# Optimization experiments

Measured on AMD Instinct MI355X. Metric: run time of the kernel, lower is better.

## Reference

```python
import jax, jax.numpy as jnp
import numpy as np

B, S_T, S_S, P, D = 4, 8, 4, 1024, 1024
NUM_REF = 256
NUM_SHARED = 256
TOPK = 4
TEMP = 1.0
STUDENT_FRAMES = [0, 2, 4, 6]          # teacher indices used by student
EXTRA_FRAMES = [1, 3, 5, 7]            # teacher-only frames
SHARED_TEACHER = [2, 4, 6]             # shared frames (student_frame_indices[1:])
W_D1 = W_D2 = W_D3 = 1.0
HUBER_OUTER_BETA = 0.5


def setup_inputs() -> dict:
    key = jax.random.key(0)
    k1, k2, k3, k4 = jax.random.split(key, 4)
    teacher_feats = jax.random.normal(k1, (B, S_T, P, D), dtype=jnp.float32)
    student_feats = jax.random.normal(k2, (B, S_S, P, D), dtype=jnp.float32)
    ref_perm = jax.random.randint(k3, (NUM_REF,), 0, P, dtype=jnp.int32)
    shared_perm = jax.random.randint(k4, (NUM_SHARED,), 0, P, dtype=jnp.int32)
    return {"teacher_feats": teacher_feats, "student_feats": student_feats,
            "ref_perm": ref_perm, "shared_perm": shared_perm}


def _l2_normalize(x, eps=1e-12):
    n = jnp.maximum(jnp.linalg.norm(x, axis=-1, keepdims=True), eps)
    return x / n


def _smooth_l1_zero(x, beta):
    # SmoothL1Loss(x, 0) elementwise
    ax = jnp.abs(x)
    return jnp.where(ax < beta, 0.5 * ax * ax / beta, ax - 0.5 * beta)


def _kl_branch(diff_t, diff_s):
    # KL(softmax(diff_t/T) || softmax(diff_s/T)) over last dim, then outer huber vs 0
    log_p = jax.nn.log_softmax(diff_t / TEMP, axis=-1)
    log_q = jax.nn.log_softmax(diff_s / TEMP, axis=-1)
    kl = jnp.sum(jnp.exp(log_p) * (log_p - log_q), axis=-1)
    return jnp.sum(_smooth_l1_zero(kl, HUBER_OUTER_BETA)), kl.size


def reference(teacher_feats, student_feats, ref_perm, shared_perm):
    sg = jax.lax.stop_gradient
    N = min(NUM_REF, NUM_SHARED)

    # ref frame (teacher idx 0 -> student idx 0), subsampled patches
    ref_t = sg(teacher_feats[:, 0][:, ref_perm, :])          # [B, num_ref, D]
    ref_s = student_feats[:, 0][:, ref_perm, :]

    # teacher-only frames concatenated along patch dim: [B, 4*P, D]
    extra_t = sg(teacher_feats[:, jnp.array(EXTRA_FRAMES)].reshape(B, len(EXTRA_FRAMES) * P, D))

    # cosine-similarity top-k search (selection_mode='topk')
    sim = jnp.einsum('bnd,bmd->bnm', _l2_normalize(ref_t), _l2_normalize(extra_t))
    _, topk_idx = jax.lax.top_k(sim, TOPK)                    # [B, num_ref, topk]
    sim_high = jax.vmap(lambda e, i: e[i])(extra_t, topk_idx)  # [B, num_ref, topk, D]
    sim_high = sg(sim_high)

    rt = ref_t[:, :N, :]
    rs = ref_s[:, :N, :]
    sh = sim_high[:, :N, :, :]

    sum_d1 = jnp.float32(0.0); sum_d2 = jnp.float32(0.0); sum_d3 = jnp.float32(0.0)
    n_d1 = 0; n_d2 = 0; n_d3 = 0

    for t_idx in SHARED_TEACHER:
        s_idx = STUDENT_FRAMES.index(t_idx)
        st = sg(teacher_feats[:, t_idx][:, shared_perm[:N], :])   # [B, N, D]
        ss = student_feats[:, s_idx][:, shared_perm[:N], :]

        # d1: ref - shared
        l1, c1 = _kl_branch(rt - st, rs - ss)
        sum_d1 += l1; n_d1 += c1
        # d2: ref - sim_high
        l2, c2 = _kl_branch(rt[:, :, None, :] - sh, rs[:, :, None, :] - sh)
        sum_d2 += l2; n_d2 += c2
        # d3: shared - sim_high
        l3, c3 = _kl_branch(st[:, :, None, :] - sh, ss[:, :, None, :] - sh)
        sum_d3 += l3; n_d3 += c3

    loss = (W_D1 * sum_d1 / n_d1 + W_D2 * sum_d2 / n_d2 + W_D3 * sum_d3 / n_d3)
    return loss
```

## Files before the change

kernel.cpp:

```cpp
#include <hip/hip_runtime.h>
#include <hip/hip_bf16.h>
#include <math.h>

#define BATCH 4

typedef __bf16 bf16x8 __attribute__((ext_vector_type(8)));
typedef float f32x4 __attribute__((ext_vector_type(4)));

#define LDSTRIDE 40

__global__ __launch_bounds__(256) void convert_kernel(const float* __restrict__ teacher,
                                                      const int* __restrict__ ref_perm,
                                                      __bf16* __restrict__ Abf,
                                                      __bf16* __restrict__ Bbf,
                                                      float* __restrict__ invnorm,
                                                      float* __restrict__ acc) {
    int blk = blockIdx.x;
    int b = blk / 4352;
    int r = blk - b * 4352;
    int t = threadIdx.x;
    if (blk == 0 && t < 4) acc[t] = 0.f;
    const float* src;
    __bf16* dst;
    bool isB = (r >= 256);
    if (!isB) {
        src = teacher + (((size_t)b * 8 + 0) * 1024 + ref_perm[r]) * 1024;
        dst = Abf + ((size_t)b * 256 + r) * 1024;
    } else {
        int m = r - 256;
        int frame = 1 + 2 * (m >> 10), p = m & 1023;
        src = teacher + (((size_t)b * 8 + frame) * 1024 + p) * 1024;
        dst = Bbf + ((size_t)b * 4096 + m) * 1024;
    }
    float4 v = ((const float4*)src)[t];
    float scale = 1.0f;
    __shared__ float red[4];
    if (isB) {
        float s = v.x * v.x + v.y * v.y + v.z * v.z + v.w * v.w;
        for (int o = 32; o > 0; o >>= 1) s += __shfl_xor(s, o);
        if ((t & 63) == 0) red[t >> 6] = s;
        __syncthreads();
        float tot = red[0] + red[1] + red[2] + red[3];
        scale = 1.0f / fmaxf(sqrtf(tot), 1e-12f);
        if (t == 0) invnorm[b * 4096 + (r - 256)] = scale;
    }
    __bf16 o4[4] = {(__bf16)(v.x * scale), (__bf16)(v.y * scale),
                    (__bf16)(v.z * scale), (__bf16)(v.w * scale)};
    ((uint2*)dst)[t] = *(uint2*)o4;
}

__global__ __launch_bounds__(512) void mfma_gemm_kernel(const __bf16* __restrict__ Abf,
                                                        const __bf16* __restrict__ Bbf,
                                                        __bf16* __restrict__ scoresb) {
    int mt = blockIdx.x;
    int nt = blockIdx.y;
    int b  = blockIdx.z;
    int t = threadIdx.x;
    int lane = t & 63, wave = t >> 6;
    int wn0 = (wave & 1) * 64;
    int wm0 = (wave >> 1) * 32;
    int l15 = lane & 15, l4 = lane >> 4;

    __shared__ __bf16 As[128 * LDSTRIDE];
    __shared__ __bf16 Bs[128 * LDSTRIDE];

    const __bf16* Ab = Abf + ((size_t)b * 256 + nt * 128) * 1024;
    const __bf16* Bb = Bbf + ((size_t)b * 4096 + mt * 128) * 1024;

    int row0 = t >> 2, kc0 = t & 3;

    f32x4 acc[4][2] = {};

    for (int k0 = 0; k0 < 1024; k0 += 32) {
        uint4 a0 = *(const uint4*)(Ab + (size_t)row0 * 1024 + k0 + kc0 * 8);
        uint4 b0 = *(const uint4*)(Bb + (size_t)row0 * 1024 + k0 + kc0 * 8);
        __syncthreads();
        *(uint4*)(As + row0 * LDSTRIDE + kc0 * 8) = a0;
        *(uint4*)(Bs + row0 * LDSTRIDE + kc0 * 8) = b0;
        __syncthreads();
        bf16x8 af[4], bfr[2];
#pragma unroll
        for (int i = 0; i < 4; i++)
            af[i] = *(const bf16x8*)(As + (wn0 + i * 16 + l15) * LDSTRIDE + l4 * 8);
#pragma unroll
        for (int j = 0; j < 2; j++)
            bfr[j] = *(const bf16x8*)(Bs + (wm0 + j * 16 + l15) * LDSTRIDE + l4 * 8);
#pragma unroll
        for (int i = 0; i < 4; i++)
#pragma unroll
            for (int j = 0; j < 2; j++)
                acc[i][j] = __builtin_amdgcn_mfma_f32_16x16x32_bf16(af[i], bfr[j], acc[i][j], 0, 0, 0);
    }

    __bf16* outp = scoresb + ((size_t)b * 256 + nt * 128) * 4096 + (size_t)mt * 128;
#pragma unroll
    for (int i = 0; i < 4; i++)
#pragma unroll
        for (int j = 0; j < 2; j++)
#pragma unroll
            for (int r = 0; r < 4; r++) {
                int n = wn0 + i * 16 + l4 * 4 + r;
                int m = wm0 + j * 16 + l15;
                outp[(size_t)n * 4096 + m] = (__bf16)acc[i][j][r];
            }
}

__global__ __launch_bounds__(256) void topk_rescore_kernel(const __bf16* __restrict__ scoresb,
                                                           const float* __restrict__ teacher,
                                                           const int* __restrict__ ref_perm,
                                                           const float* __restrict__ invnorm,
                                                           int* __restrict__ topk) {
    int row = blockIdx.x;
    int b = row >> 8, n = row & 255;
    int t = threadIdx.x;
    int lane = t & 63, wave = t >> 6;

    __shared__ float refr[1024];
    __shared__ float cval[32];
    __shared__ int cidx[32];
    __shared__ int cand_i[8];
    __shared__ float exact_v[8];

    const float* Tb = teacher + (size_t)b * 8 * 1024 * 1024;
    int rp = ref_perm[n];
    ((float4*)refr)[t] = ((const float4*)(Tb + (size_t)rp * 1024))[t];

    const __bf16* srow = scoresb + (size_t)row * 4096;
    __bf16 xs[16];
    *(uint4*)xs = ((const uint4*)srow)[2 * t];
    *(uint4*)(xs + 8) = ((const uint4*)srow)[2 * t + 1];

    float v[8]; int ix[8];
#pragma unroll
    for (int i = 0; i < 8; i++) { v[i] = -1e38f; ix[i] = -1; }
#pragma unroll
    for (int jj = 0; jj < 16; jj++) {
        float xv = (float)xs[jj]; int xm = t * 16 + jj;
        if (xv > v[7]) {
            v[7] = xv; ix[7] = xm;
#pragma unroll
            for (int i = 7; i > 0; i--)
                if (v[i] > v[i - 1]) {
                    float tv = v[i]; v[i] = v[i - 1]; v[i - 1] = tv;
                    int ti = ix[i]; ix[i] = ix[i - 1]; ix[i - 1] = ti;
                }
        }
    }
    for (int r = 0; r < 8; r++) {
        float bv = v[0]; int bi = ix[0];
        for (int o = 32; o > 0; o >>= 1) {
            float ov = __shfl_xor(bv, o); int oi = __shfl_xor(bi, o);
            if (ov > bv || (ov == bv && oi > bi)) { bv = ov; bi = oi; }
        }
        if (lane == 0) { cval[wave * 8 + r] = bv; cidx[wave * 8 + r] = bi; }
        if (bi == ix[0]) {
            v[0] = v[1]; ix[0] = ix[1];
            v[1] = v[2]; ix[1] = ix[2];
            v[2] = v[3]; ix[2] = ix[3];
            v[3] = v[4]; ix[3] = ix[4];
            v[4] = v[5]; ix[4] = ix[5];
            v[5] = v[6]; ix[5] = ix[6];
            v[6] = v[7]; ix[6] = ix[7];
            v[7] = -1e38f; ix[7] = -1;
        }
    }
    __syncthreads();
    if (wave == 0) {
        float mv = (lane < 32) ? cval[lane] : -1e38f;
        int mi = (lane < 32) ? cidx[lane] : -1;
        for (int r = 0; r < 8; r++) {
            float bv = mv; int bi = mi;
            for (int o = 32; o > 0; o >>= 1) {
                float ov = __shfl_xor(bv, o); int oi = __shfl_xor(bi, o);
                if (ov > bv || (ov == bv && oi > bi)) { bv = ov; bi = oi; }
            }
            if (lane == 0) cand_i[r] = bi;
            if (bi == mi) mv = -1e38f;
        }
    }
    __syncthreads();
    for (int c = wave; c < 8; c += 4) {
        int m = cand_i[c];
        int frame = 1 + 2 * (m >> 10), p = m & 1023;
        const float* ext = Tb + ((size_t)frame * 1024 + p) * 1024;
        float s = 0.f;
#pragma unroll
        for (int jj = 0; jj < 16; jj++) {
            int d = lane + 64 * jj;
            s = fmaf(refr[d], ext[d], s);
        }
        for (int o = 32; o > 0; o >>= 1) s += __shfl_xor(s, o);
        if (lane == 0) exact_v[c] = s * invnorm[b * 4096 + m];
    }
    __syncthreads();
    if (t == 0) {
        unsigned used = 0;
        for (int r = 0; r < 4; r++) {
            float bv = -1e38f; int bc = 0;
            for (int c = 0; c < 8; c++)
                if (!(used & (1u << c)) && exact_v[c] > bv) { bv = exact_v[c]; bc = c; }
            used |= 1u << bc;
            topk[row * 4 + r] = cand_i[bc];
        }
    }
}

#define RT 0
#define RS 1024
#define ST 2048
#define SS 3072
#define SH 4096
__global__ __launch_bounds__(256) void kl_kernel(const float* __restrict__ teacher,
                                                 const float* __restrict__ student,
                                                 const int* __restrict__ ref_perm,
                                                 const int* __restrict__ shared_perm,
                                                 const int* __restrict__ topk,
                                                 float* __restrict__ acc) {
    int row = blockIdx.x;
    int ti  = blockIdx.y;
    int b = row >> 8;
    int n = row & 255;
    int t = threadIdx.x;
    int lane = t & 63, wave = t >> 6;

    __shared__ float buf[8192];
    __shared__ float res3[3];
    if (t < 3) res3[t] = 0.f;

    const float* Tb = teacher + (size_t)b * 8 * 1024 * 1024;
    const float* Sb = student + (size_t)b * 4 * 1024 * 1024;

    int rp = ref_perm[n];
    int sp = shared_perm[n];
    int t_idx = 2 * ti + 2;
    int s_idx = ti + 1;
    ((float4*)(buf + RT))[t] = ((const float4*)(Tb + (size_t)rp * 1024))[t];
    ((float4*)(buf + RS))[t] = ((const float4*)(Sb + (size_t)rp * 1024))[t];
    ((float4*)(buf + ST))[t] = ((const float4*)(Tb + ((size_t)t_idx * 1024 + sp) * 1024))[t];
    ((float4*)(buf + SS))[t] = ((const float4*)(Sb + ((size_t)s_idx * 1024 + sp) * 1024))[t];
#pragma unroll
    for (int k = 0; k < 4; k++) {
        int idx = topk[row * 4 + k];
        int frame = 1 + 2 * (idx >> 10), p = idx & 1023;
        ((float4*)(buf + SH + k * 1024))[t] = ((const float4*)(Tb + ((size_t)frame * 1024 + p) * 1024))[t];
    }
    __syncthreads();

    int nrows = (ti == 0) ? 9 : 5;
    for (int idx = wave; idx < nrows; idx += 4) {
        int r = (ti == 0) ? idx : (idx == 0 ? 0 : idx + 4);
        int at, bt, as, bs, branch;
        float w;
        if (r == 0)      { at = RT; bt = ST;                 as = RS; bs = SS; branch = 0; w = 1.f; }
        else if (r < 5)  { at = RT; bt = SH + (r - 1) * 1024; as = RS; bs = bt; branch = 1; w = 3.f; }
        else             { at = ST; bt = SH + (r - 5) * 1024; as = SS; bs = bt; branch = 2; w = 1.f; }

        float dt[16], ds[16];
        float mt = -1e38f, ms = -1e38f;
#pragma unroll
        for (int j = 0; j < 16; j++) {
            int d = lane + 64 * j;
            float av = buf[at + d], bv = buf[bt + d];
            float asv = buf[as + d], bsv = buf[bs + d];
            dt[j] = av - bv;
            ds[j] = asv - bsv;
            mt = fmaxf(mt, dt[j]);
            ms = fmaxf(ms, ds[j]);
        }
        for (int o = 32; o > 0; o >>= 1) {
            mt = fmaxf(mt, __shfl_xor(mt, o));
            ms = fmaxf(ms, __shfl_xor(ms, o));
        }
        float Zt = 0.f, Zs = 0.f, Tn = 0.f;
#pragma unroll
        for (int j = 0; j < 16; j++) {
            float et = __expf(dt[j] - mt);
            Zt += et;
            Zs += __expf(ds[j] - ms);
            Tn += et * (dt[j] - ds[j]);
        }
        for (int o = 32; o > 0; o >>= 1) {
            Zt += __shfl_xor(Zt, o);
            Zs += __shfl_xor(Zs, o);
            Tn += __shfl_xor(Tn, o);
        }
        if (lane == 0) {
            float kl = Tn / Zt - mt - __logf(Zt) + ms + __logf(Zs);
            float ax = fabsf(kl);
            float h = ax < 0.5f ? ax * ax : ax - 0.25f;
            atomicAdd(&res3[branch], h * w);
        }
    }
    __syncthreads();
    if (t < 3) atomicAdd(&acc[t], res3[t]);
}

__global__ void finalize_kernel(const float* __restrict__ acc, float* __restrict__ out) {
    out[0] = acc[0] / 3072.f + acc[1] / 12288.f + acc[2] / 12288.f;
}

extern "C" void kernel_launch(void* const* d_in, const int* in_sizes, int n_in,
                              void* d_out, int out_size, void* d_ws, size_t ws_size,
                              hipStream_t stream) {
    const float* teacher = (const float*)d_in[0];
    const float* student = (const float*)d_in[1];
    const int* ref_perm = (const int*)d_in[2];
    const int* shared_perm = (const int*)d_in[3];
    float* out = (float*)d_out;

    char* ws = (char*)d_ws;
    float* acc     = (float*)ws;
    float* invnorm = (float*)(ws + 64);
    int*   topk    = (int*)(ws + 64 + 65536);
    __bf16* Abf    = (__bf16*)(ws + 64 + 65536 + 16384);
    __bf16* Bbf    = Abf + (size_t)4 * 256 * 1024;
    __bf16* scoresb = Bbf + (size_t)4 * 4096 * 1024;

    convert_kernel<<<BATCH * 4352, 256, 0, stream>>>(teacher, ref_perm, Abf, Bbf, invnorm, acc);
    mfma_gemm_kernel<<<dim3(32, 2, 4), 512, 0, stream>>>(Abf, Bbf, scoresb);
    topk_rescore_kernel<<<1024, 256, 0, stream>>>(scoresb, teacher, ref_perm, invnorm, topk);
    kl_kernel<<<dim3(1024, 3), 256, 0, stream>>>(teacher, student, ref_perm, shared_perm, topk, acc);
    finalize_kernel<<<1, 1, 0, stream>>>(acc, out);
}
```

Before: 293.9 us.

## Fuse d2 KL branch into top-k kernel and enlarge per-wave GEMM tile

The d2 (ref minus sim_high) KL terms depend only on the ref row and its top-k neighbours, not on the shared frame. They are now computed once in the top-k kernel, using the already-loaded ref rows and weighted by 3, instead of being recomputed by the ti==0 slice of the KL kernel. That slice previously did 9 rows per block against 5 for the others, so the KL kernel becomes uniform. The GEMM also moves from 512 to 256 threads, with each wave computing a 64x64 tile (16 MFMA accumulators) and each thread loading two chunks. This gives more register reuse per LDS read but fewer waves to hide latency.

```diff
diff --git a/kernel.cpp b/kernel.cpp
--- a/kernel.cpp
+++ b/kernel.cpp
@@ -49,7 +49,7 @@
     ((uint2*)dst)[t] = *(uint2*)o4;
 }
 
-__global__ __launch_bounds__(512) void mfma_gemm_kernel(const __bf16* __restrict__ Abf,
+__global__ __launch_bounds__(256) void mfma_gemm_kernel(const __bf16* __restrict__ Abf,
                                                         const __bf16* __restrict__ Bbf,
                                                         __bf16* __restrict__ scoresb) {
     int mt = blockIdx.x;
@@ -58,7 +58,7 @@
     int t = threadIdx.x;
     int lane = t & 63, wave = t >> 6;
     int wn0 = (wave & 1) * 64;
-    int wm0 = (wave >> 1) * 32;
+    int wm0 = (wave >> 1) * 64;
     int l15 = lane & 15, l4 = lane >> 4;
 
     __shared__ __bf16 As[128 * LDSTRIDE];
@@ -67,28 +67,33 @@
     const __bf16* Ab = Abf + ((size_t)b * 256 + nt * 128) * 1024;
     const __bf16* Bb = Bbf + ((size_t)b * 4096 + mt * 128) * 1024;
 
-    int row0 = t >> 2, kc0 = t & 3;
-
-    f32x4 acc[4][2] = {};
+    int e0 = t, e1 = t + 256;
+    int row0 = e0 >> 2, kc0 = e0 & 3;
+    int row1 = e1 >> 2, kc1 = e1 & 3;
+
+    f32x4 acc[4][4] = {};
 
     for (int k0 = 0; k0 < 1024; k0 += 32) {
         uint4 a0 = *(const uint4*)(Ab + (size_t)row0 * 1024 + k0 + kc0 * 8);
+        uint4 a1 = *(const uint4*)(Ab + (size_t)row1 * 1024 + k0 + kc1 * 8);
         uint4 b0 = *(const uint4*)(Bb + (size_t)row0 * 1024 + k0 + kc0 * 8);
+        uint4 b1 = *(const uint4*)(Bb + (size_t)row1 * 1024 + k0 + kc1 * 8);
         __syncthreads();
         *(uint4*)(As + row0 * LDSTRIDE + kc0 * 8) = a0;
+        *(uint4*)(As + row1 * LDSTRIDE + kc1 * 8) = a1;
         *(uint4*)(Bs + row0 * LDSTRIDE + kc0 * 8) = b0;
+        *(uint4*)(Bs + row1 * LDSTRIDE + kc1 * 8) = b1;
         __syncthreads();
-        bf16x8 af[4], bfr[2];
+        bf16x8 af[4], bfr[4];
+#pragma unroll
+        for (int i = 0; i < 4; i++) {
+            af[i]  = *(const bf16x8*)(As + (wn0 + i * 16 + l15) * LDSTRIDE + l4 * 8);
+            bfr[i] = *(const bf16x8*)(Bs + (wm0 + i * 16 + l15) * LDSTRIDE + l4 * 8);
+        }
 #pragma unroll
         for (int i = 0; i < 4; i++)
-            af[i] = *(const bf16x8*)(As + (wn0 + i * 16 + l15) * LDSTRIDE + l4 * 8);
-#pragma unroll
-        for (int j = 0; j < 2; j++)
-            bfr[j] = *(const bf16x8*)(Bs + (wm0 + j * 16 + l15) * LDSTRIDE + l4 * 8);
-#pragma unroll
-        for (int i = 0; i < 4; i++)
-#pragma unroll
-            for (int j = 0; j < 2; j++)
+#pragma unroll
+            for (int j = 0; j < 4; j++)
                 acc[i][j] = __builtin_amdgcn_mfma_f32_16x16x32_bf16(af[i], bfr[j], acc[i][j], 0, 0, 0);
     }
 
@@ -96,7 +101,7 @@
 #pragma unroll
     for (int i = 0; i < 4; i++)
 #pragma unroll
-        for (int j = 0; j < 2; j++)
+        for (int j = 0; j < 4; j++)
 #pragma unroll
             for (int r = 0; r < 4; r++) {
                 int n = wn0 + i * 16 + l4 * 4 + r;
@@ -105,25 +110,30 @@
             }
 }
 
-__global__ __launch_bounds__(256) void topk_rescore_kernel(const __bf16* __restrict__ scoresb,
-                                                           const float* __restrict__ teacher,
-                                                           const int* __restrict__ ref_perm,
-                                                           const float* __restrict__ invnorm,
-                                                           int* __restrict__ topk) {
+__global__ __launch_bounds__(256) void topk_d2_kernel(const __bf16* __restrict__ scoresb,
+                                                      const float* __restrict__ teacher,
+                                                      const float* __restrict__ student,
+                                                      const int* __restrict__ ref_perm,
+                                                      const float* __restrict__ invnorm,
+                                                      int* __restrict__ topk,
+                                                      float* __restrict__ acc) {
     int row = blockIdx.x;
     int b = row >> 8, n = row & 255;
     int t = threadIdx.x;
     int lane = t & 63, wave = t >> 6;
 
-    __shared__ float refr[1024];
+    __shared__ float refr[1024], refs[1024];
     __shared__ float cval[32];
     __shared__ int cidx[32];
     __shared__ int cand_i[8];
     __shared__ float exact_v[8];
+    __shared__ int wm4[4];
 
     const float* Tb = teacher + (size_t)b * 8 * 1024 * 1024;
+    const float* Sb = student + (size_t)b * 4 * 1024 * 1024;
     int rp = ref_perm[n];
     ((float4*)refr)[t] = ((const float4*)(Tb + (size_t)rp * 1024))[t];
+    ((float4*)refs)[t] = ((const float4*)(Sb + (size_t)rp * 1024))[t];
 
     const __bf16* srow = scoresb + (size_t)row * 4096;
     __bf16 xs[16];
@@ -200,7 +210,48 @@
             for (int c = 0; c < 8; c++)
                 if (!(used & (1u << c)) && exact_v[c] > bv) { bv = exact_v[c]; bc = c; }
             used |= 1u << bc;
+            wm4[r] = cand_i[bc];
             topk[row * 4 + r] = cand_i[bc];
+        }
+    }
+    __syncthreads();
+    {
+        int m = wm4[wave];
+        int frame = 1 + 2 * (m >> 10), p = m & 1023;
+        const float* shr = Tb + ((size_t)frame * 1024 + p) * 1024;
+        float dt[16], ds[16];
+        float mt = -1e38f, ms = -1e38f;
+#pragma unroll
+        for (int j = 0; j < 16; j++) {
+            int d = lane + 64 * j;
+            float sv = shr[d];
+            dt[j] = refr[d] - sv;
+            ds[j] = refs[d] - sv;
+            mt = fmaxf(mt, dt[j]);
+            ms = fmaxf(ms, ds[j]);
+        }
+        for (int o = 32; o > 0; o >>= 1) {
+            mt = fmaxf(mt, __shfl_xor(mt, o));
+            ms = fmaxf(ms, __shfl_xor(ms, o));
+        }
+        float Zt = 0.f, Zs = 0.f, Tn = 0.f;
+#pragma unroll
+        for (int j = 0; j < 16; j++) {
+            float et = __expf(dt[j] - mt);
+            Zt += et;
+            Zs += __expf(ds[j] - ms);
+            Tn += et * (dt[j] - ds[j]);
+        }
+        for (int o = 32; o > 0; o >>= 1) {
+            Zt += __shfl_xor(Zt, o);
+            Zs += __shfl_xor(Zs, o);
+            Tn += __shfl_xor(Tn, o);
+        }
+        if (lane == 0) {
+            float kl = Tn / Zt - mt - __logf(Zt) + ms + __logf(Zs);
+            float ax = fabsf(kl);
+            float h = ax < 0.5f ? ax * ax : ax - 0.25f;
+            atomicAdd(&acc[1], h * 3.0f);
         }
     }
 }
@@ -224,8 +275,8 @@
     int lane = t & 63, wave = t >> 6;
 
     __shared__ float buf[8192];
-    __shared__ float res3[3];
-    if (t < 3) res3[t] = 0.f;
+    __shared__ float res2[2];
+    if (t < 2) res2[t] = 0.f;
 
     const float* Tb = teacher + (size_t)b * 8 * 1024 * 1024;
     const float* Sb = student + (size_t)b * 4 * 1024 * 1024;
@@ -246,14 +297,10 @@
     }
     __syncthreads();
 
-    int nrows = (ti == 0) ? 9 : 5;
-    for (int idx = wave; idx < nrows; idx += 4) {
-        int r = (ti == 0) ? idx : (idx == 0 ? 0 : idx + 4);
+    for (int r = wave; r < 5; r += 4) {
         int at, bt, as, bs, branch;
-        float w;
-        if (r == 0)      { at = RT; bt = ST;                 as = RS; bs = SS; branch = 0; w = 1.f; }
-        else if (r < 5)  { at = RT; bt = SH + (r - 1) * 1024; as = RS; bs = bt; branch = 1; w = 3.f; }
-        else             { at = ST; bt = SH + (r - 5) * 1024; as = SS; bs = bt; branch = 2; w = 1.f; }
+        if (r == 0) { at = RT; bt = ST;                 as = RS; bs = SS; branch = 0; }
+        else        { at = ST; bt = SH + (r - 1) * 1024; as = SS; bs = bt; branch = 1; }
 
         float dt[16], ds[16];
         float mt = -1e38f, ms = -1e38f;
@@ -288,11 +335,12 @@
             float kl = Tn / Zt - mt - __logf(Zt) + ms + __logf(Zs);
             float ax = fabsf(kl);
             float h = ax < 0.5f ? ax * ax : ax - 0.25f;
-            atomicAdd(&res3[branch], h * w);
-        }
-    }
-    __syncthreads();
-    if (t < 3) atomicAdd(&acc[t], res3[t]);
+            atomicAdd(&res2[branch], h);
+        }
+    }
+    __syncthreads();
+    if (t == 0) atomicAdd(&acc[0], res2[0]);
+    if (t == 1) atomicAdd(&acc[2], res2[1]);
 }
 
 __global__ void finalize_kernel(const float* __restrict__ acc, float* __restrict__ out) {
@@ -317,8 +365,8 @@
     __bf16* scoresb = Bbf + (size_t)4 * 4096 * 1024;
 
     convert_kernel<<<BATCH * 4352, 256, 0, stream>>>(teacher, ref_perm, Abf, Bbf, invnorm, acc);
-    mfma_gemm_kernel<<<dim3(32, 2, 4), 512, 0, stream>>>(Abf, Bbf, scoresb);
-    topk_rescore_kernel<<<1024, 256, 0, stream>>>(scoresb, teacher, ref_perm, invnorm, topk);
+    mfma_gemm_kernel<<<dim3(32, 2, 4), 256, 0, stream>>>(Abf, Bbf, scoresb);
+    topk_d2_kernel<<<1024, 256, 0, stream>>>(scoresb, teacher, student, ref_perm, invnorm, topk, acc);
     kl_kernel<<<dim3(1024, 3), 256, 0, stream>>>(teacher, student, ref_perm, shared_perm, topk, acc);
     finalize_kernel<<<1, 1, 0, stream>>>(acc, out);
 }
```

Result: slower. 381.8 us (+29.9%).
